# Optimization experiments

Measured on AMD Instinct MI355X. Metric: run time of the kernel, lower is better.

The kernel has to match this reference:

```python
import jax, jax.numpy as jnp
import numpy as np

XMIN, XMAX = -16.0, 16.0
ZMIN, ZMAX = -16.0, 16.0
SOFTCLIP_L = 5.0


def ref2mem(traj, Zs, Xs):
    # traj: (B, T, 2) cam (x, z) -> mem pixel coords
    x = (traj[..., 0] - XMIN) / ((XMAX - XMIN) / Xs) - 0.5
    z = (traj[..., 1] - ZMIN) / ((ZMAX - ZMIN) / Zs) - 0.5
    return x, z


def bilinear_sample2d(pm, x, z):
    # pm: (B, C, Z, X); x, z: (B, N) float coords -> (B, C, N)
    B, C, Zs, Xs = pm.shape
    x = jnp.clip(x, 0.0, Xs - 1.0)
    z = jnp.clip(z, 0.0, Zs - 1.0)
    x0 = jnp.floor(x).astype(jnp.int32)
    z0 = jnp.floor(z).astype(jnp.int32)
    x1 = jnp.minimum(x0 + 1, Xs - 1)
    z1 = jnp.minimum(z0 + 1, Zs - 1)
    wx = x - x0.astype(x.dtype)
    wz = z - z0.astype(z.dtype)
    pm_flat = pm.reshape(B, C, Zs * Xs)

    def gather(zi, xi):
        idx = (zi * Xs + xi)[:, None, :]  # (B,1,N)
        return jnp.take_along_axis(pm_flat, jnp.broadcast_to(idx, (B, C, idx.shape[-1])), axis=2)

    v00 = gather(z0, x0); v01 = gather(z0, x1)
    v10 = gather(z1, x0); v11 = gather(z1, x1)
    wx = wx[:, None, :]; wz = wz[:, None, :]
    return (v00 * (1 - wx) * (1 - wz) + v01 * wx * (1 - wz)
            + v10 * (1 - wx) * wz + v11 * wx * wz)


def gru_cell(x, h, W_ih, W_hh, b_ih, b_hh):
    gi = x @ W_ih.T + b_ih
    gh = h @ W_hh.T + b_hh
    i_r, i_z, i_n = jnp.split(gi, 3, axis=1)
    h_r, h_z, h_n = jnp.split(gh, 3, axis=1)
    r = jax.nn.sigmoid(i_r + h_r)
    z = jax.nn.sigmoid(i_z + h_z)
    n = jnp.tanh(i_n + r * h_n)
    return (1.0 - z) * n + z * h


def expm_softclip(sig_raw):
    B = sig_raw.shape[0]
    nrm = jnp.linalg.norm(sig_raw.reshape(B, -1), axis=1)
    denom = jax.nn.logsumexp(jnp.stack([nrm / SOFTCLIP_L, jnp.ones_like(nrm)], axis=-1), axis=-1)
    return sig_raw / denom[:, None, None]


def reference(feat_map, pred_map, noise, traj_past,
              W_ih, W_hh, b_ih, b_hh, past_W, past_b,
              W1, b1, W2, b2, W3, b3):
    B, C, Zf, Xf = feat_map.shape
    Zp, Xp = pred_map.shape[2], pred_map.shape[3]
    T_futu = noise.shape[1]
    H = W_hh.shape[1]
    eye2 = jnp.eye(2, dtype=feat_map.dtype)

    # static feature: max_pool2d k=8 s=8 + past encoding
    pooled = feat_map.reshape(B, C, Zf // 8, 8, Xf // 8, 8).max(axis=(3, 5)).reshape(B, -1)
    past_enc = traj_past.reshape(B, -1) @ past_W.T + past_b
    sta_feat = jnp.concatenate([pooled, past_enc], axis=1)  # (B, 2080)

    def step(carry, noise_t):
        hx, win = carry
        xm, zm = ref2mem(win, Zp, Xp)
        feats = bilinear_sample2d(pred_map, xm, zm).reshape(B, -1)  # (B, 3)
        dyn_feat = jnp.concatenate([feats, win.reshape(B, -1)], axis=1)  # (B, 9)
        hx = gru_cell(dyn_feat, hx, W_ih, W_hh, b_ih, b_hh)
        joint = jnp.concatenate([hx, sta_feat], axis=1)  # (B, 2112)
        h1 = jax.nn.leaky_relu(joint @ W1.T + b1)
        h2 = jax.nn.leaky_relu(h1 @ W2.T + b2)
        pred = h2 @ W3.T + b3  # (B, 6)
        mu = pred[:, :2]
        sig_raw = pred[:, 2:].reshape(B, 2, 2) + 1e-8 * eye2
        sig_raw = expm_softclip(sig_raw)
        sig = jnp.einsum('bij,bkj->bik', sig_raw, sig_raw)
        xdotdot = mu + jnp.sum(sig * noise_t[:, None, :], axis=1)
        x_next = 2.0 * win[:, -1] - win[:, -2] + xdotdot  # verlet, dt=1
        win = jnp.concatenate([win[:, 1:], x_next[:, None]], axis=1)
        return (hx, win), x_next

    hx0 = jnp.zeros((B, H), dtype=feat_map.dtype)
    (_, _), traj_futu = jax.lax.scan(step, (hx0, traj_past), jnp.swapaxes(noise, 0, 1))
    return jnp.swapaxes(traj_futu, 0, 1)  # (B, T_futu, 2)


def setup_inputs():
    key = jax.random.key(0)
    ks = jax.random.split(key, 16)
    B, C, Zf, Xf = 192, 32, 64, 64
    T_futu, T_past, H = 27, 3, 32
    d = {}
    d['feat_map'] = jax.random.normal(ks[0], (B, C, Zf, Xf), jnp.float32)
    d['pred_map'] = jax.random.normal(ks[1], (B, 1, Zf, Xf), jnp.float32)
    d['noise'] = jax.random.normal(ks[2], (B, T_futu, 2), jnp.float32)
    d['traj_past'] = jax.random.normal(ks[3], (B, T_past, 2), jnp.float32) * 4.0
    s = 0.05
    d['W_ih'] = jax.random.normal(ks[4], (3 * H, 9), jnp.float32) * s
    d['W_hh'] = jax.random.normal(ks[5], (3 * H, H), jnp.float32) * s
    d['b_ih'] = jnp.zeros((3 * H,), jnp.float32)
    d['b_hh'] = jnp.zeros((3 * H,), jnp.float32)
    d['past_W'] = jax.random.normal(ks[6], (32, T_past * 2), jnp.float32) * s
    d['past_b'] = jnp.zeros((32,), jnp.float32)
    d['W1'] = jax.random.normal(ks[7], (64, 2112), jnp.float32) * 0.02
    d['b1'] = jnp.zeros((64,), jnp.float32)
    d['W2'] = jax.random.normal(ks[8], (32, 64), jnp.float32) * s
    d['b2'] = jnp.zeros((32,), jnp.float32)
    d['W3'] = jax.random.normal(ks[9], (6, 32), jnp.float32) * s
    d['b3'] = jnp.zeros((6,), jnp.float32)
    return d
```

## Files before the change

### kernel.cpp

```cpp
#include <hip/hip_runtime.h>
#include <hip/hip_bf16.h>
#include <math.h>

typedef unsigned int u32;
typedef __fp16 f16x2 __attribute__((ext_vector_type(2)));

#define NB    192
#define NC    32
#define TFUT  27

#if __has_builtin(__builtin_amdgcn_rcpf)
#define RCPF(x) __builtin_amdgcn_rcpf(x)
#else
#define RCPF(x) (1.0f / (x))
#endif
#if __has_builtin(__builtin_amdgcn_sqrtf)
#define SQRTF(x) __builtin_amdgcn_sqrtf(x)
#else
#define SQRTF(x) sqrtf(x)
#endif
#if __has_builtin(__builtin_amdgcn_exp2f)
#define EXP2F(x) __builtin_amdgcn_exp2f(x)
#else
#define EXP2F(x) exp2f(x)
#endif
#if __has_builtin(__builtin_amdgcn_logf)
#define LOG2F(x) __builtin_amdgcn_logf(x)
#else
#define LOG2F(x) log2f(x)
#endif

__device__ __forceinline__ u32 pk16(float lo, float hi) {
    auto v = __builtin_amdgcn_cvt_pkrtz(lo, hi);
    return __builtin_bit_cast(u32, v);
}
__device__ __forceinline__ float fdot2pk(u32 a, u32 b, float c) {
#if __has_builtin(__builtin_amdgcn_fdot2)
    return __builtin_amdgcn_fdot2(__builtin_bit_cast(f16x2, a),
                                  __builtin_bit_cast(f16x2, b), c, false);
#else
    f16x2 av = __builtin_bit_cast(f16x2, a), bv = __builtin_bit_cast(f16x2, b);
    return c + (float)av[0] * (float)bv[0] + (float)av[1] * (float)bv[1];
#endif
}
__device__ __forceinline__ float swz_xor1(float v) {
    return __int_as_float(__builtin_amdgcn_ds_swizzle(__float_as_int(v), 0x041F));
}
__device__ __forceinline__ u32 rdl(u32 v, int lane) {
    return (u32)__builtin_amdgcn_readlane((int)v, lane);
}
__device__ __forceinline__ float rdlf(float v, int lane) {
    return __int_as_float(__builtin_amdgcn_readlane(__float_as_int(v), lane));
}
__device__ __forceinline__ float sigmoid_f(float x) {
    return RCPF(1.0f + EXP2F(-1.4426950408889634f * x));
}
__device__ __forceinline__ float tanh_f(float x) {
    return __builtin_fmaf(2.0f, RCPF(1.0f + EXP2F(-2.8853900817779268f * x)), -1.0f);
}

__global__ __launch_bounds__(1024) void k_static(
    const float* __restrict__ feat,
    const float* __restrict__ traj_past,
    const float* __restrict__ past_W,
    const float* __restrict__ past_b,
    const float* __restrict__ W1,
    const float* __restrict__ b1,
    float* __restrict__ sta1)
{
    __shared__ __align__(16) float sta[2080];
    const int b = blockIdx.x;
    const int t = threadIdx.x;

    for (int it = 0; it < 2; ++it) {
        const int c    = it * 16 + (t >> 6);
        const int cell = t & 63;
        const int zi = cell >> 3, xi = cell & 7;
        const float* p = feat + ((size_t)b * NC + c) * 4096 + zi * 8 * 64 + xi * 8;
        float m = -3.402823466e38f;
        #pragma unroll
        for (int dz = 0; dz < 8; ++dz) {
            const float4 v0 = *reinterpret_cast<const float4*>(p + dz * 64);
            const float4 v1 = *reinterpret_cast<const float4*>(p + dz * 64 + 4);
            m = fmaxf(m, fmaxf(fmaxf(fmaxf(v0.x, v0.y), fmaxf(v0.z, v0.w)),
                               fmaxf(fmaxf(v1.x, v1.y), fmaxf(v1.z, v1.w))));
        }
        sta[c * 64 + cell] = m;
    }
    if (t < 32) {
        float acc = past_b[t];
        #pragma unroll
        for (int k = 0; k < 6; ++k) acc += past_W[t * 6 + k] * traj_past[b * 6 + k];
        sta[2048 + t] = acc;
    }
    __syncthreads();

    const int o = t >> 4, l = t & 15;
    const float* wrow = W1 + (size_t)o * 2112 + 32;
    float acc = 0.f;
    #pragma unroll 4
    for (int j = 0; j < 32; ++j) {
        const int k = j * 64 + l * 4;
        const float4 w = *reinterpret_cast<const float4*>(wrow + k);
        const float4 s = *reinterpret_cast<const float4*>(&sta[k]);
        acc += w.x * s.x + w.y * s.y + w.z * s.z + w.w * s.w;
    }
    if (l < 8) {
        const int k = 2048 + l * 4;
        const float4 w = *reinterpret_cast<const float4*>(wrow + k);
        const float4 s = *reinterpret_cast<const float4*>(&sta[k]);
        acc += w.x * s.x + w.y * s.y + w.z * s.z + w.w * s.w;
    }
    acc += __shfl_xor(acc, 1);
    acc += __shfl_xor(acc, 2);
    acc += __shfl_xor(acc, 4);
    acc += __shfl_xor(acc, 8);
    if (l == 0) sta1[b * 64 + o] = b1[o] + acc;
}

__global__ __launch_bounds__(64, 1) void k_recur(
    const float* __restrict__ pred_map,
    const float* __restrict__ noise,
    const float* __restrict__ traj_past,
    const float* __restrict__ W_ih,
    const float* __restrict__ W_hh,
    const float* __restrict__ b_ih,
    const float* __restrict__ b_hh,
    const float* __restrict__ W1,
    const float* __restrict__ W2,
    const float* __restrict__ b2,
    const float* __restrict__ W3,
    const float* __restrict__ b3,
    const float* __restrict__ sta1g,
    float* __restrict__ out)
{
    __shared__ __align__(16) float pm[4096];
    __shared__ __align__(8)  float nz[56];

    const int b = blockIdx.x;
    const int l = threadIdx.x;
    const int m = l & 31;

    {
        const float4* src = reinterpret_cast<const float4*>(pred_map + (size_t)b * 4096);
        float4* dst = reinterpret_cast<float4*>(pm);
        #pragma unroll
        for (int i = 0; i < 16; ++i) dst[l + i * 64] = src[l + i * 64];
    }
    if (l < TFUT * 2) nz[l] = noise[b * (TFUT * 2) + l];

    float wih[9], wih2[9];
    #pragma unroll
    for (int k = 0; k < 9; ++k) {
        wih[k]  = W_ih[l * 9 + k];
        wih2[k] = W_ih[(64 + m) * 9 + k];
    }
    u32 whhp[16], whh2p[16], w1ap[16], w2p[32], w3p[16];
    #pragma unroll
    for (int j = 0; j < 16; ++j)
        whhp[j]  = pk16(W_hh[l * 32 + 2*j],        W_hh[l * 32 + 2*j + 1]);
    #pragma unroll
    for (int j = 0; j < 16; ++j)
        whh2p[j] = pk16(W_hh[(64 + m) * 32 + 2*j], W_hh[(64 + m) * 32 + 2*j + 1]);
    #pragma unroll
    for (int j = 0; j < 16; ++j)
        w1ap[j]  = pk16(W1[(size_t)l * 2112 + 2*j], W1[(size_t)l * 2112 + 2*j + 1]);
    #pragma unroll
    for (int j = 0; j < 32; ++j)
        w2p[j]   = pk16(W2[m * 64 + 2*j],          W2[m * 64 + 2*j + 1]);
    const int wr = (l < 6) ? l : 0;
    #pragma unroll
    for (int j = 0; j < 16; ++j)
        w3p[j]   = pk16(W3[wr * 32 + 2*j],         W3[wr * 32 + 2*j + 1]);

    const float bihl = b_ih[l], bhhl = b_hh[l];
    const float bih2 = b_ih[64 + m], bhh2 = b_hh[64 + m];
    const float b2l  = b2[m];
    float b3r[6];
    #pragma unroll
    for (int r = 0; r < 6; ++r) b3r[r] = b3[r];
    const float sta1l = sta1g[b * 64 + l];

    float w[6];
    #pragma unroll
    for (int j = 0; j < 6; ++j) w[j] = traj_past[b * 6 + j];
    float hxloc = 0.f;
    u32 hxpk[16];
    #pragma unroll
    for (int j = 0; j < 16; ++j) hxpk[j] = 0u;

    __syncthreads();

    auto bsample = [&](float px, float pz) -> float {
        float x = (px + 16.0f) * 2.0f - 0.5f;
        float z = (pz + 16.0f) * 2.0f - 0.5f;
        x = fminf(fmaxf(x, 0.0f), 63.0f);
        z = fminf(fmaxf(z, 0.0f), 63.0f);
        const float xf = floorf(x), zf = floorf(z);
        const int x0 = (int)xf, z0 = (int)zf;
        const int x1 = min(x0 + 1, 63), z1 = min(z0 + 1, 63);
        const float wx = x - xf, wz = z - zf;
        const float v00 = pm[z0 * 64 + x0], v01 = pm[z0 * 64 + x1];
        const float v10 = pm[z1 * 64 + x0], v11 = pm[z1 * 64 + x1];
        return v00 * (1.f - wx) * (1.f - wz) + v01 * wx * (1.f - wz)
             + v10 * (1.f - wx) * wz        + v11 * wx * wz;
    };
    float s0 = bsample(w[0], w[1]);
    float s1 = bsample(w[2], w[3]);
    float s2 = bsample(w[4], w[5]);

    const bool odd = (l & 1);

    for (int ts = 0; ts < TFUT; ++ts) {
        const float2 nn = *reinterpret_cast<const float2*>(&nz[2 * ts]);

        float gi = bihl + wih[0] * s0 + wih[1] * s1 + wih[2] * s2;
        #pragma unroll
        for (int j = 0; j < 6; ++j) gi += wih[3 + j] * w[j];
        float gi2 = bih2 + wih2[0] * s0 + wih2[1] * s1 + wih2[2] * s2;
        #pragma unroll
        for (int j = 0; j < 6; ++j) gi2 += wih2[3 + j] * w[j];

        float A0 = 0.f, A1 = 0.f, A2 = 0.f, A3 = 0.f;
        float C0 = 0.f, C1 = 0.f, C2 = 0.f, C3 = 0.f;
        #pragma unroll
        for (int j = 0; j < 16; j += 4) {
            A0 = fdot2pk(hxpk[j],   whhp[j],   A0);
            A1 = fdot2pk(hxpk[j+1], whhp[j+1], A1);
            A2 = fdot2pk(hxpk[j+2], whhp[j+2], A2);
            A3 = fdot2pk(hxpk[j+3], whhp[j+3], A3);
            C0 = fdot2pk(hxpk[j],   whh2p[j],   C0);
            C1 = fdot2pk(hxpk[j+1], whh2p[j+1], C1);
            C2 = fdot2pk(hxpk[j+2], whh2p[j+2], C2);
            C3 = fdot2pk(hxpk[j+3], whh2p[j+3], C3);
        }
        const float gs  = gi  + bhhl + ((A0 + A1) + (A2 + A3));
        const float gh2 = bhh2 + ((C0 + C1) + (C2 + C3));

        const float sg = sigmoid_f(gs);
        const float zv = __shfl_xor(sg, 32, 64);
        const float nv = tanh_f(gi2 + sg * gh2);
        const float hnew = (1.0f - zv) * nv + zv * hxloc;
        hxloc = hnew;

        {
            const float nb = swz_xor1(hnew);
            const float plo = odd ? nb : hnew;
            const float phi = odd ? hnew : nb;
            const u32 hpk = pk16(plo, phi);
            #pragma unroll
            for (int j = 0; j < 16; ++j) hxpk[j] = rdl(hpk, 2 * j);
        }

        float D0 = 0.f, D1 = 0.f, D2 = 0.f, D3 = 0.f;
        #pragma unroll
        for (int j = 0; j < 16; j += 4) {
            D0 = fdot2pk(hxpk[j],   w1ap[j],   D0);
            D1 = fdot2pk(hxpk[j+1], w1ap[j+1], D1);
            D2 = fdot2pk(hxpk[j+2], w1ap[j+2], D2);
            D3 = fdot2pk(hxpk[j+3], w1ap[j+3], D3);
        }
        const float h1a = sta1l + ((D0 + D1) + (D2 + D3));
        const float h1l = (h1a >= 0.f) ? h1a : 0.01f * h1a;

        u32 h1pk[32];
        {
            const float nb = swz_xor1(h1l);
            const float plo = odd ? nb : h1l;
            const float phi = odd ? h1l : nb;
            const u32 hpk = pk16(plo, phi);
            #pragma unroll
            for (int j = 0; j < 32; ++j) h1pk[j] = rdl(hpk, 2 * j);
        }

        float P0 = 0.f, P1 = 0.f, P2 = 0.f, P3 = 0.f;
        #pragma unroll
        for (int j = 0; j < 32; j += 4) {
            P0 = fdot2pk(h1pk[j],   w2p[j],   P0);
            P1 = fdot2pk(h1pk[j+1], w2p[j+1], P1);
            P2 = fdot2pk(h1pk[j+2], w2p[j+2], P2);
            P3 = fdot2pk(h1pk[j+3], w2p[j+3], P3);
        }
        const float h2a = b2l + ((P0 + P1) + (P2 + P3));
        const float h2l = (h2a >= 0.f) ? h2a : 0.01f * h2a;

        u32 h2pk[16];
        {
            const float nb = swz_xor1(h2l);
            const float plo = odd ? nb : h2l;
            const float phi = odd ? h2l : nb;
            const u32 hpk = pk16(plo, phi);
            #pragma unroll
            for (int j = 0; j < 16; ++j) h2pk[j] = rdl(hpk, 2 * j);
        }
        float Q0 = 0.f, Q1 = 0.f, Q2 = 0.f, Q3 = 0.f;
        #pragma unroll
        for (int j = 0; j < 16; j += 4) {
            Q0 = fdot2pk(h2pk[j],   w3p[j],   Q0);
            Q1 = fdot2pk(h2pk[j+1], w3p[j+1], Q1);
            Q2 = fdot2pk(h2pk[j+2], w3p[j+2], Q2);
            Q3 = fdot2pk(h2pk[j+3], w3p[j+3], Q3);
        }
        const float praw = ((Q0 + Q1) + (Q2 + Q3));

        const float pv0 = rdlf(praw, 0) + b3r[0];
        const float pv1 = rdlf(praw, 1) + b3r[1];
        const float pv2 = rdlf(praw, 2) + b3r[2];
        const float pv3 = rdlf(praw, 3) + b3r[3];
        const float pv4 = rdlf(praw, 4) + b3r[4];
        const float pv5 = rdlf(praw, 5) + b3r[5];

        float s00 = pv2 + 1e-8f, s01 = pv3;
        float s10 = pv4,          s11 = pv5 + 1e-8f;
        const float nrm = SQRTF(s00 * s00 + s01 * s01 + s10 * s10 + s11 * s11);
        const float arg = nrm * 0.2f;
        const float mm  = fmaxf(arg, 1.0f);
        const float d   = fabsf(arg - 1.0f);
        const float denom = mm + 0.6931471805599453f *
                            LOG2F(1.0f + EXP2F(-1.4426950408889634f * d));
        const float inv = RCPF(denom);
        s00 *= inv; s01 *= inv; s10 *= inv; s11 *= inv;
        const float sig00 = s00 * s00 + s01 * s01;
        const float sig01 = s00 * s10 + s01 * s11;
        const float sig11 = s10 * s10 + s11 * s11;
        const float xd0 = pv0 + nn.x * (sig00 + sig01);
        const float xd1 = pv1 + nn.y * (sig01 + sig11);
        const float nx0 = 2.0f * w[4] - w[2] + xd0;
        const float nx1 = 2.0f * w[5] - w[3] + xd1;

        if (l == 0) {
            float2 o; o.x = nx0; o.y = nx1;
            *reinterpret_cast<float2*>(out + ((size_t)b * TFUT + ts) * 2) = o;
        }

        w[0] = w[2]; w[1] = w[3];
        w[2] = w[4]; w[3] = w[5];
        w[4] = nx0;  w[5] = nx1;
        s0 = s1; s1 = s2;
        s2 = bsample(nx0, nx1);
    }
}

extern "C" void kernel_launch(void* const* d_in, const int* in_sizes, int n_in,
                              void* d_out, int out_size, void* d_ws, size_t ws_size,
                              hipStream_t stream) {
    const float* feat      = (const float*)d_in[0];
    const float* pred_map  = (const float*)d_in[1];
    const float* noise     = (const float*)d_in[2];
    const float* traj_past = (const float*)d_in[3];
    const float* W_ih      = (const float*)d_in[4];
    const float* W_hh      = (const float*)d_in[5];
    const float* b_ih      = (const float*)d_in[6];
    const float* b_hh      = (const float*)d_in[7];
    const float* past_W    = (const float*)d_in[8];
    const float* past_b    = (const float*)d_in[9];
    const float* W1        = (const float*)d_in[10];
    const float* b1        = (const float*)d_in[11];
    const float* W2        = (const float*)d_in[12];
    const float* b2        = (const float*)d_in[13];
    const float* W3        = (const float*)d_in[14];
    const float* b3        = (const float*)d_in[15];
    float* outp = (float*)d_out;
    float* sta1 = (float*)d_ws;

    k_static<<<dim3(NB), dim3(1024), 0, stream>>>(feat, traj_past, past_W, past_b, W1, b1, sta1);
    k_recur<<<dim3(NB), dim3(64), 0, stream>>>(pred_map, noise, traj_past,
                                               W_ih, W_hh, b_ih, b_hh,
                                               W1, W2, b2, W3, b3, sta1, outp);
}
```

Before: 49.70 us.

## Prepack recurrent weights into a workspace blob and shorten GRU critical path

An extra block in the static kernel pre-packs all per-lane GRU/MLP weights and biases into a contiguous 128-word blob per lane, so the recurrent kernel loads them with 32 vector loads instead of many scattered scalar loads plus fp16 conversions. The hidden-state dot products are moved to right after h is updated, so the next step's recurrent term is precomputed off the gate critical path. Lane-pair packing switches from ds_swizzle with select to a DPP quad-permute. The cost is one extra block in the first kernel and extra workspace traffic.

```diff
diff --git a/kernel.cpp b/kernel.cpp
--- a/kernel.cpp
+++ b/kernel.cpp
@@ -4,10 +4,12 @@
 
 typedef unsigned int u32;
 typedef __fp16 f16x2 __attribute__((ext_vector_type(2)));
+typedef u32 u32x4 __attribute__((ext_vector_type(4)));
 
 #define NB    192
 #define NC    32
 #define TFUT  27
+#define BLOB_F_OFF (NB * 64)
 
 #if __has_builtin(__builtin_amdgcn_rcpf)
 #define RCPF(x) __builtin_amdgcn_rcpf(x)
@@ -43,14 +45,15 @@
     return c + (float)av[0] * (float)bv[0] + (float)av[1] * (float)bv[1];
 #endif
 }
-__device__ __forceinline__ float swz_xor1(float v) {
-    return __int_as_float(__builtin_amdgcn_ds_swizzle(__float_as_int(v), 0x041F));
-}
 __device__ __forceinline__ u32 rdl(u32 v, int lane) {
     return (u32)__builtin_amdgcn_readlane((int)v, lane);
 }
 __device__ __forceinline__ float rdlf(float v, int lane) {
     return __int_as_float(__builtin_amdgcn_readlane(__float_as_int(v), lane));
+}
+__device__ __forceinline__ float dpp_xor1(float v) {
+    return __int_as_float(__builtin_amdgcn_update_dpp(
+        0, __float_as_int(v), 0xB1, 0xF, 0xF, true));
 }
 __device__ __forceinline__ float sigmoid_f(float x) {
     return RCPF(1.0f + EXP2F(-1.4426950408889634f * x));
@@ -66,11 +69,53 @@
     const float* __restrict__ past_b,
     const float* __restrict__ W1,
     const float* __restrict__ b1,
-    float* __restrict__ sta1)
+    const float* __restrict__ W_ih,
+    const float* __restrict__ W_hh,
+    const float* __restrict__ b_ih,
+    const float* __restrict__ b_hh,
+    const float* __restrict__ W2,
+    const float* __restrict__ b2,
+    const float* __restrict__ W3,
+    const float* __restrict__ b3,
+    float* __restrict__ ws)
 {
-    __shared__ __align__(16) float sta[2080];
     const int b = blockIdx.x;
     const int t = threadIdx.x;
+
+    if (b == NB) {
+        if (t >= 64) return;
+        const int l = t, m2 = l & 31;
+        u32* blob = reinterpret_cast<u32*>(ws) + BLOB_F_OFF + (size_t)l * 128;
+        #pragma unroll
+        for (int k = 0; k < 9; ++k) {
+            blob[k]     = __float_as_uint(W_ih[l * 9 + k]);
+            blob[9 + k] = __float_as_uint(W_ih[(64 + m2) * 9 + k]);
+        }
+        #pragma unroll
+        for (int j = 0; j < 16; ++j) {
+            blob[18 + j] = pk16(W_hh[l * 32 + 2*j],          W_hh[l * 32 + 2*j + 1]);
+            blob[34 + j] = pk16(W_hh[(64 + m2) * 32 + 2*j],  W_hh[(64 + m2) * 32 + 2*j + 1]);
+            blob[50 + j] = pk16(W1[(size_t)l * 2112 + 2*j],  W1[(size_t)l * 2112 + 2*j + 1]);
+        }
+        #pragma unroll
+        for (int j = 0; j < 32; ++j)
+            blob[66 + j] = pk16(W2[m2 * 64 + 2*j], W2[m2 * 64 + 2*j + 1]);
+        const int wr = (l < 6) ? l : 0;
+        #pragma unroll
+        for (int j = 0; j < 16; ++j)
+            blob[98 + j] = pk16(W3[wr * 32 + 2*j], W3[wr * 32 + 2*j + 1]);
+        blob[114] = __float_as_uint(b_ih[l]);
+        blob[115] = __float_as_uint(b_hh[l]);
+        blob[116] = __float_as_uint(b_ih[64 + m2]);
+        blob[117] = __float_as_uint(b_hh[64 + m2]);
+        blob[118] = __float_as_uint(b2[m2]);
+        #pragma unroll
+        for (int r = 0; r < 6; ++r) blob[119 + r] = __float_as_uint(b3[r]);
+        blob[125] = blob[126] = blob[127] = 0u;
+        return;
+    }
+
+    __shared__ __align__(16) float sta[2080];
 
     for (int it = 0; it < 2; ++it) {
         const int c    = it * 16 + (t >> 6);
@@ -115,23 +160,14 @@
     acc += __shfl_xor(acc, 2);
     acc += __shfl_xor(acc, 4);
     acc += __shfl_xor(acc, 8);
-    if (l == 0) sta1[b * 64 + o] = b1[o] + acc;
+    if (l == 0) ws[b * 64 + o] = b1[o] + acc;
 }
 
 __global__ __launch_bounds__(64, 1) void k_recur(
     const float* __restrict__ pred_map,
     const float* __restrict__ noise,
     const float* __restrict__ traj_past,
-    const float* __restrict__ W_ih,
-    const float* __restrict__ W_hh,
-    const float* __restrict__ b_ih,
-    const float* __restrict__ b_hh,
-    const float* __restrict__ W1,
-    const float* __restrict__ W2,
-    const float* __restrict__ b2,
-    const float* __restrict__ W3,
-    const float* __restrict__ b3,
-    const float* __restrict__ sta1g,
+    const float* __restrict__ ws,
     float* __restrict__ out)
 {
     __shared__ __align__(16) float pm[4096];
@@ -139,7 +175,6 @@
 
     const int b = blockIdx.x;
     const int l = threadIdx.x;
-    const int m = l & 31;
 
     {
         const float4* src = reinterpret_cast<const float4*>(pred_map + (size_t)b * 4096);
@@ -149,37 +184,15 @@
     }
     if (l < TFUT * 2) nz[l] = noise[b * (TFUT * 2) + l];
 
-    float wih[9], wih2[9];
-    #pragma unroll
-    for (int k = 0; k < 9; ++k) {
-        wih[k]  = W_ih[l * 9 + k];
-        wih2[k] = W_ih[(64 + m) * 9 + k];
-    }
-    u32 whhp[16], whh2p[16], w1ap[16], w2p[32], w3p[16];
-    #pragma unroll
-    for (int j = 0; j < 16; ++j)
-        whhp[j]  = pk16(W_hh[l * 32 + 2*j],        W_hh[l * 32 + 2*j + 1]);
-    #pragma unroll
-    for (int j = 0; j < 16; ++j)
-        whh2p[j] = pk16(W_hh[(64 + m) * 32 + 2*j], W_hh[(64 + m) * 32 + 2*j + 1]);
-    #pragma unroll
-    for (int j = 0; j < 16; ++j)
-        w1ap[j]  = pk16(W1[(size_t)l * 2112 + 2*j], W1[(size_t)l * 2112 + 2*j + 1]);
+    const u32* blob = reinterpret_cast<const u32*>(ws) + BLOB_F_OFF + (size_t)l * 128;
+    u32x4 dv[32];
     #pragma unroll
     for (int j = 0; j < 32; ++j)
-        w2p[j]   = pk16(W2[m * 64 + 2*j],          W2[m * 64 + 2*j + 1]);
-    const int wr = (l < 6) ? l : 0;
-    #pragma unroll
-    for (int j = 0; j < 16; ++j)
-        w3p[j]   = pk16(W3[wr * 32 + 2*j],         W3[wr * 32 + 2*j + 1]);
-
-    const float bihl = b_ih[l], bhhl = b_hh[l];
-    const float bih2 = b_ih[64 + m], bhh2 = b_hh[64 + m];
-    const float b2l  = b2[m];
-    float b3r[6];
-    #pragma unroll
-    for (int r = 0; r < 6; ++r) b3r[r] = b3[r];
-    const float sta1l = sta1g[b * 64 + l];
+        dv[j] = reinterpret_cast<const u32x4*>(blob)[j];
+#define DW(i) (dv[(i) >> 2][(i) & 3])
+#define DF(i) __int_as_float((int)DW(i))
+
+    const float sta1l = ws[b * 64 + l];
 
     float w[6];
     #pragma unroll
@@ -188,6 +201,7 @@
     u32 hxpk[16];
     #pragma unroll
     for (int j = 0; j < 16; ++j) hxpk[j] = 0u;
+    float Adot = 0.f, Cdot = 0.f;
 
     __syncthreads();
 
@@ -209,115 +223,108 @@
     float s1 = bsample(w[2], w[3]);
     float s2 = bsample(w[4], w[5]);
 
-    const bool odd = (l & 1);
-
     for (int ts = 0; ts < TFUT; ++ts) {
         const float2 nn = *reinterpret_cast<const float2*>(&nz[2 * ts]);
 
-        float gi = bihl + wih[0] * s0 + wih[1] * s1 + wih[2] * s2;
-        #pragma unroll
-        for (int j = 0; j < 6; ++j) gi += wih[3 + j] * w[j];
-        float gi2 = bih2 + wih2[0] * s0 + wih2[1] * s1 + wih2[2] * s2;
-        #pragma unroll
-        for (int j = 0; j < 6; ++j) gi2 += wih2[3 + j] * w[j];
-
-        float A0 = 0.f, A1 = 0.f, A2 = 0.f, A3 = 0.f;
-        float C0 = 0.f, C1 = 0.f, C2 = 0.f, C3 = 0.f;
-        #pragma unroll
-        for (int j = 0; j < 16; j += 4) {
-            A0 = fdot2pk(hxpk[j],   whhp[j],   A0);
-            A1 = fdot2pk(hxpk[j+1], whhp[j+1], A1);
-            A2 = fdot2pk(hxpk[j+2], whhp[j+2], A2);
-            A3 = fdot2pk(hxpk[j+3], whhp[j+3], A3);
-            C0 = fdot2pk(hxpk[j],   whh2p[j],   C0);
-            C1 = fdot2pk(hxpk[j+1], whh2p[j+1], C1);
-            C2 = fdot2pk(hxpk[j+2], whh2p[j+2], C2);
-            C3 = fdot2pk(hxpk[j+3], whh2p[j+3], C3);
-        }
-        const float gs  = gi  + bhhl + ((A0 + A1) + (A2 + A3));
-        const float gh2 = bhh2 + ((C0 + C1) + (C2 + C3));
-
+        float gi  = DF(114) + DF(3) * w[0] + DF(4) * w[1] + DF(5) * w[2]
+                            + DF(6) * w[3] + DF(7) * w[4] + DF(8) * w[5];
+        float gi2 = DF(116) + DF(12) * w[0] + DF(13) * w[1] + DF(14) * w[2]
+                            + DF(15) * w[3] + DF(16) * w[4] + DF(17) * w[5];
+        gi  += DF(0) * s0 + DF(1) * s1 + DF(2) * s2;
+        gi2 += DF(9) * s0 + DF(10) * s1 + DF(11) * s2;
+
+        const float gs   = gi + DF(115) + Adot;
+        const float gh2v = DF(117) + Cdot;
         const float sg = sigmoid_f(gs);
         const float zv = __shfl_xor(sg, 32, 64);
-        const float nv = tanh_f(gi2 + sg * gh2);
+        const float nv = tanh_f(gi2 + sg * gh2v);
         const float hnew = (1.0f - zv) * nv + zv * hxloc;
         hxloc = hnew;
 
+        const u32 hpk = pk16(hnew, dpp_xor1(hnew));
+        #pragma unroll
+        for (int j = 0; j < 16; ++j) hxpk[j] = rdl(hpk, 2 * j);
+
         {
-            const float nb = swz_xor1(hnew);
-            const float plo = odd ? nb : hnew;
-            const float phi = odd ? hnew : nb;
-            const u32 hpk = pk16(plo, phi);
+            float A0 = 0.f, A1 = 0.f, A2 = 0.f, A3 = 0.f;
+            float C0 = 0.f, C1 = 0.f, C2 = 0.f, C3 = 0.f;
             #pragma unroll
-            for (int j = 0; j < 16; ++j) hxpk[j] = rdl(hpk, 2 * j);
+            for (int j = 0; j < 16; j += 4) {
+                A0 = fdot2pk(hxpk[j],   DW(18 + j),     A0);
+                A1 = fdot2pk(hxpk[j+1], DW(18 + j + 1), A1);
+                A2 = fdot2pk(hxpk[j+2], DW(18 + j + 2), A2);
+                A3 = fdot2pk(hxpk[j+3], DW(18 + j + 3), A3);
+                C0 = fdot2pk(hxpk[j],   DW(34 + j),     C0);
+                C1 = fdot2pk(hxpk[j+1], DW(34 + j + 1), C1);
+                C2 = fdot2pk(hxpk[j+2], DW(34 + j + 2), C2);
+                C3 = fdot2pk(hxpk[j+3], DW(34 + j + 3), C3);
+            }
+            Adot = (A0 + A1) + (A2 + A3);
+            Cdot = (C0 + C1) + (C2 + C3);
         }
 
         float D0 = 0.f, D1 = 0.f, D2 = 0.f, D3 = 0.f;
         #pragma unroll
         for (int j = 0; j < 16; j += 4) {
-            D0 = fdot2pk(hxpk[j],   w1ap[j],   D0);
-            D1 = fdot2pk(hxpk[j+1], w1ap[j+1], D1);
-            D2 = fdot2pk(hxpk[j+2], w1ap[j+2], D2);
-            D3 = fdot2pk(hxpk[j+3], w1ap[j+3], D3);
+            D0 = fdot2pk(hxpk[j],   DW(50 + j),     D0);
+            D1 = fdot2pk(hxpk[j+1], DW(50 + j + 1), D1);
+            D2 = fdot2pk(hxpk[j+2], DW(50 + j + 2), D2);
+            D3 = fdot2pk(hxpk[j+3], DW(50 + j + 3), D3);
         }
         const float h1a = sta1l + ((D0 + D1) + (D2 + D3));
         const float h1l = (h1a >= 0.f) ? h1a : 0.01f * h1a;
 
+        const u32 h1p = pk16(h1l, dpp_xor1(h1l));
         u32 h1pk[32];
-        {
-            const float nb = swz_xor1(h1l);
-            const float plo = odd ? nb : h1l;
-            const float phi = odd ? h1l : nb;
-            const u32 hpk = pk16(plo, phi);
-            #pragma unroll
-            for (int j = 0; j < 32; ++j) h1pk[j] = rdl(hpk, 2 * j);
-        }
+        #pragma unroll
+        for (int j = 0; j < 32; ++j) h1pk[j] = rdl(h1p, 2 * j);
 
         float P0 = 0.f, P1 = 0.f, P2 = 0.f, P3 = 0.f;
-        #pragma unroll
-        for (int j = 0; j < 32; j += 4) {
-            P0 = fdot2pk(h1pk[j],   w2p[j],   P0);
-            P1 = fdot2pk(h1pk[j+1], w2p[j+1], P1);
-            P2 = fdot2pk(h1pk[j+2], w2p[j+2], P2);
-            P3 = fdot2pk(h1pk[j+3], w2p[j+3], P3);
-        }
-        const float h2a = b2l + ((P0 + P1) + (P2 + P3));
+        float P4 = 0.f, P5 = 0.f, P6 = 0.f, P7 = 0.f;
+        #pragma unroll
+        for (int j = 0; j < 32; j += 8) {
+            P0 = fdot2pk(h1pk[j],   DW(66 + j),     P0);
+            P1 = fdot2pk(h1pk[j+1], DW(66 + j + 1), P1);
+            P2 = fdot2pk(h1pk[j+2], DW(66 + j + 2), P2);
+            P3 = fdot2pk(h1pk[j+3], DW(66 + j + 3), P3);
+            P4 = fdot2pk(h1pk[j+4], DW(66 + j + 4), P4);
+            P5 = fdot2pk(h1pk[j+5], DW(66 + j + 5), P5);
+            P6 = fdot2pk(h1pk[j+6], DW(66 + j + 6), P6);
+            P7 = fdot2pk(h1pk[j+7], DW(66 + j + 7), P7);
+        }
+        const float h2a = DF(118) + (((P0 + P1) + (P2 + P3)) + ((P4 + P5) + (P6 + P7)));
         const float h2l = (h2a >= 0.f) ? h2a : 0.01f * h2a;
 
+        const u32 h2p = pk16(h2l, dpp_xor1(h2l));
         u32 h2pk[16];
-        {
-            const float nb = swz_xor1(h2l);
-            const float plo = odd ? nb : h2l;
-            const float phi = odd ? h2l : nb;
-            const u32 hpk = pk16(plo, phi);
-            #pragma unroll
-            for (int j = 0; j < 16; ++j) h2pk[j] = rdl(hpk, 2 * j);
-        }
+        #pragma unroll
+        for (int j = 0; j < 16; ++j) h2pk[j] = rdl(h2p, 2 * j);
+
         float Q0 = 0.f, Q1 = 0.f, Q2 = 0.f, Q3 = 0.f;
         #pragma unroll
         for (int j = 0; j < 16; j += 4) {
-            Q0 = fdot2pk(h2pk[j],   w3p[j],   Q0);
-            Q1 = fdot2pk(h2pk[j+1], w3p[j+1], Q1);
-            Q2 = fdot2pk(h2pk[j+2], w3p[j+2], Q2);
-            Q3 = fdot2pk(h2pk[j+3], w3p[j+3], Q3);
-        }
-        const float praw = ((Q0 + Q1) + (Q2 + Q3));
-
-        const float pv0 = rdlf(praw, 0) + b3r[0];
-        const float pv1 = rdlf(praw, 1) + b3r[1];
-        const float pv2 = rdlf(praw, 2) + b3r[2];
-        const float pv3 = rdlf(praw, 3) + b3r[3];
-        const float pv4 = rdlf(praw, 4) + b3r[4];
-        const float pv5 = rdlf(praw, 5) + b3r[5];
+            Q0 = fdot2pk(h2pk[j],   DW(98 + j),     Q0);
+            Q1 = fdot2pk(h2pk[j+1], DW(98 + j + 1), Q1);
+            Q2 = fdot2pk(h2pk[j+2], DW(98 + j + 2), Q2);
+            Q3 = fdot2pk(h2pk[j+3], DW(98 + j + 3), Q3);
+        }
+        const float praw = (Q0 + Q1) + (Q2 + Q3);
+
+        const float pv0 = rdlf(praw, 0) + DF(119);
+        const float pv1 = rdlf(praw, 1) + DF(120);
+        const float pv2 = rdlf(praw, 2) + DF(121);
+        const float pv3 = rdlf(praw, 3) + DF(122);
+        const float pv4 = rdlf(praw, 4) + DF(123);
+        const float pv5 = rdlf(praw, 5) + DF(124);
 
         float s00 = pv2 + 1e-8f, s01 = pv3;
         float s10 = pv4,          s11 = pv5 + 1e-8f;
         const float nrm = SQRTF(s00 * s00 + s01 * s01 + s10 * s10 + s11 * s11);
         const float arg = nrm * 0.2f;
         const float mm  = fmaxf(arg, 1.0f);
-        const float d   = fabsf(arg - 1.0f);
+        const float dd  = fabsf(arg - 1.0f);
         const float denom = mm + 0.6931471805599453f *
-                            LOG2F(1.0f + EXP2F(-1.4426950408889634f * d));
+                            LOG2F(1.0f + EXP2F(-1.4426950408889634f * dd));
         const float inv = RCPF(denom);
         s00 *= inv; s01 *= inv; s10 *= inv; s11 *= inv;
         const float sig00 = s00 * s00 + s01 * s01;
@@ -339,6 +346,8 @@
         s0 = s1; s1 = s2;
         s2 = bsample(nx0, nx1);
     }
+#undef DW
+#undef DF
 }
 
 extern "C" void kernel_launch(void* const* d_in, const int* in_sizes, int n_in,
@@ -361,10 +370,10 @@
     const float* W3        = (const float*)d_in[14];
     const float* b3        = (const float*)d_in[15];
     float* outp = (float*)d_out;
-    float* sta1 = (float*)d_ws;
-
-    k_static<<<dim3(NB), dim3(1024), 0, stream>>>(feat, traj_past, past_W, past_b, W1, b1, sta1);
-    k_recur<<<dim3(NB), dim3(64), 0, stream>>>(pred_map, noise, traj_past,
-                                               W_ih, W_hh, b_ih, b_hh,
-                                               W1, W2, b2, W3, b3, sta1, outp);
-}
+    float* ws   = (float*)d_ws;
+
+    k_static<<<dim3(NB + 1), dim3(1024), 0, stream>>>(
+        feat, traj_past, past_W, past_b, W1, b1,
+        W_ih, W_hh, b_ih, b_hh, W2, b2, W3, b3, ws);
+    k_recur<<<dim3(NB), dim3(64), 0, stream>>>(pred_map, noise, traj_past, ws, outp);
+}
```

New measurement: 47.18 us. 5.1% less time.
